# Performance work log

Hardware: AMD Instinct MI355X
Metric: run time of the kernel (lower is better)

## Reference

```python
import jax, jax.numpy as jnp
import numpy as np

TOTAL_NODES = 262144
NUM_GRAPHS = 1024
MAX_NODES = 512
D = 256


def setup_inputs() -> dict:
    key = jax.random.key(0)
    k1, k2 = jax.random.split(key)
    node_emb = jax.random.normal(k1, (TOTAL_NODES, D), dtype=jnp.float32)
    batch_idx = jnp.sort(jax.random.randint(k2, (TOTAL_NODES,), 0, NUM_GRAPHS, dtype=jnp.int64))
    return {"node_emb": node_emb, "batch_idx": batch_idx,
            "num_graphs": NUM_GRAPHS, "max_nodes": MAX_NODES}


def reference(node_emb, batch_idx, num_graphs, max_nodes):
    # counts[g] = number of nodes in graph g  (torch.bincount)
    n = node_emb.shape[0]
    counts = jax.ops.segment_sum(jnp.ones((n,), dtype=jnp.int32), batch_idx,
                                 num_segments=num_graphs)
    # exclusive prefix sum -> start offset of each graph's node block
    starts = jnp.cumsum(counts) - counts
    # position of each node within its graph (batch_idx is sorted)
    pos = jnp.arange(n, dtype=jnp.int32) - starts[batch_idx]
    # single fused scatter replacing the per-graph python loop
    enc_states = jnp.zeros((num_graphs, max_nodes, node_emb.shape[-1]),
                           dtype=node_emb.dtype)
    enc_states = enc_states.at[batch_idx, pos].set(node_emb)
    # mask: first counts[g] slots of each row are 1
    enc_mask = (jnp.arange(max_nodes, dtype=jnp.int32)[None, :]
                < counts[:, None]).astype(jnp.int32)
    return enc_states, enc_mask
```

## Files before the change

### kernel.cpp

```cpp
#include <hip/hip_runtime.h>

#define NUM_GRAPHS 1024
#define MAX_NODES  512
#define DIM        256
#define D4         (DIM / 4)

__global__ void compute_offsets_kernel(const int* __restrict__ bidx32, int n,
                                       int* __restrict__ starts,
                                       int* __restrict__ counts) {
    int g = blockIdx.x * blockDim.x + threadIdx.x;
    if (g >= NUM_GRAPHS) return;
    const bool is64 = (bidx32[n - 1] == 0);

    int lo = 0, hi = n;
    while (lo < hi) {
        int mid = (lo + hi) >> 1;
        int v = is64 ? bidx32[2 * mid] : bidx32[mid];
        if (v < g) lo = mid + 1; else hi = mid;
    }
    int s = lo;

    int g1 = g + 1;
    lo = 0; hi = n;
    while (lo < hi) {
        int mid = (lo + hi) >> 1;
        int v = is64 ? bidx32[2 * mid] : bidx32[mid];
        if (v < g1) lo = mid + 1; else hi = mid;
    }

    starts[g] = s;
    counts[g] = lo - s;
}

__global__ void scatter_states_kernel(const float4* __restrict__ emb,
                                      const int* __restrict__ starts,
                                      const int* __restrict__ counts,
                                      float4* __restrict__ out) {
    const int total = NUM_GRAPHS * MAX_NODES * D4;
    const int stride = gridDim.x * blockDim.x;
    for (int v = blockIdx.x * blockDim.x + threadIdx.x; v < total; v += stride) {
        int row  = v >> 6;
        int lane = v & (D4 - 1);
        int g    = row >> 9;
        int slot = row & (MAX_NODES - 1);
        float4 val = make_float4(0.f, 0.f, 0.f, 0.f);
        if (slot < counts[g]) {
            val = emb[(size_t)(starts[g] + slot) * D4 + lane];
        }
        out[v] = val;
    }
}

__global__ void mask_kernel(const int* __restrict__ counts,
                            float* __restrict__ mask) {
    int idx = blockIdx.x * blockDim.x + threadIdx.x;
    if (idx >= NUM_GRAPHS * MAX_NODES) return;
    int g    = idx >> 9;
    int slot = idx & (MAX_NODES - 1);
    mask[idx] = (slot < counts[g]) ? 1.0f : 0.0f;
}

extern "C" void kernel_launch(void* const* d_in, const int* in_sizes, int n_in,
                              void* d_out, int out_size, void* d_ws, size_t ws_size,
                              hipStream_t stream) {
    const float* node_emb = (const float*)d_in[0];
    const int*   bidx32   = (const int*)d_in[1];
    const int    n        = in_sizes[1];

    int* starts = (int*)d_ws;
    int* counts = starts + NUM_GRAPHS;

    compute_offsets_kernel<<<(NUM_GRAPHS + 255) / 256, 256, 0, stream>>>(
        bidx32, n, starts, counts);

    scatter_states_kernel<<<2048, 256, 0, stream>>>(
        (const float4*)node_emb, starts, counts, (float4*)d_out);

    float* mask = (float*)d_out + (size_t)NUM_GRAPHS * MAX_NODES * DIM;
    mask_kernel<<<(NUM_GRAPHS * MAX_NODES) / 256, 256, 0, stream>>>(counts, mask);
}
```

Before: 206.1 us.

## Fuse mask into scatter, replace binary search with boundary scan, use nontemporal IO

Replaces the per-graph binary-search offset kernel with a per-node boundary-detection kernel that writes start offsets (counts derived as differences). Folds the mask kernel into the scatter kernel, cutting one launch, and fixes the scatter loop to 64 unrolled iterations with constant stride. Uses nontemporal loads/stores for streaming embedding data to reduce cache pollution. The scan launches far more threads, and empty trailing graphs are filled serially by one thread.

After: 188.3 us. -8.6%, faster.

```diff
diff --git a/kernel.cpp b/kernel.cpp
--- a/kernel.cpp
+++ b/kernel.cpp
@@ -4,60 +4,51 @@
 #define MAX_NODES  512
 #define DIM        256
 #define D4         (DIM / 4)
+#define TOTAL_V4   (NUM_GRAPHS * MAX_NODES * D4)
+#define NTHREADS   (2048 * 256)
 
-__global__ void compute_offsets_kernel(const int* __restrict__ bidx32, int n,
-                                       int* __restrict__ starts,
-                                       int* __restrict__ counts) {
-    int g = blockIdx.x * blockDim.x + threadIdx.x;
-    if (g >= NUM_GRAPHS) return;
+typedef float f4 __attribute__((ext_vector_type(4)));
+
+__global__ void scan_offsets_kernel(const int* __restrict__ bidx32, int n,
+                                    int* __restrict__ starts) {
+    int i = blockIdx.x * blockDim.x + threadIdx.x;
+    if (i >= n) return;
     const bool is64 = (bidx32[n - 1] == 0);
-
-    int lo = 0, hi = n;
-    while (lo < hi) {
-        int mid = (lo + hi) >> 1;
-        int v = is64 ? bidx32[2 * mid] : bidx32[mid];
-        if (v < g) lo = mid + 1; else hi = mid;
-    }
-    int s = lo;
-
-    int g1 = g + 1;
-    lo = 0; hi = n;
-    while (lo < hi) {
-        int mid = (lo + hi) >> 1;
-        int v = is64 ? bidx32[2 * mid] : bidx32[mid];
-        if (v < g1) lo = mid + 1; else hi = mid;
-    }
-
-    starts[g] = s;
-    counts[g] = lo - s;
-}
-
-__global__ void scatter_states_kernel(const float4* __restrict__ emb,
-                                      const int* __restrict__ starts,
-                                      const int* __restrict__ counts,
-                                      float4* __restrict__ out) {
-    const int total = NUM_GRAPHS * MAX_NODES * D4;
-    const int stride = gridDim.x * blockDim.x;
-    for (int v = blockIdx.x * blockDim.x + threadIdx.x; v < total; v += stride) {
-        int row  = v >> 6;
-        int lane = v & (D4 - 1);
-        int g    = row >> 9;
-        int slot = row & (MAX_NODES - 1);
-        float4 val = make_float4(0.f, 0.f, 0.f, 0.f);
-        if (slot < counts[g]) {
-            val = emb[(size_t)(starts[g] + slot) * D4 + lane];
-        }
-        out[v] = val;
+    const int cur  = is64 ? bidx32[2 * i] : bidx32[i];
+    const int prev = (i == 0) ? -1 : (is64 ? bidx32[2 * (i - 1)] : bidx32[i - 1]);
+    for (int g = prev + 1; g <= cur; ++g) starts[g] = i;
+    if (i == n - 1) {
+        for (int g = cur + 1; g <= NUM_GRAPHS; ++g) starts[g] = n;
     }
 }
 
-__global__ void mask_kernel(const int* __restrict__ counts,
-                            float* __restrict__ mask) {
-    int idx = blockIdx.x * blockDim.x + threadIdx.x;
-    if (idx >= NUM_GRAPHS * MAX_NODES) return;
-    int g    = idx >> 9;
-    int slot = idx & (MAX_NODES - 1);
-    mask[idx] = (slot < counts[g]) ? 1.0f : 0.0f;
+__global__ void __launch_bounds__(256)
+scatter_states_kernel(const f4* __restrict__ emb,
+                      const int* __restrict__ starts,
+                      f4* __restrict__ out,
+                      float* __restrict__ mask) {
+    const int tid  = blockIdx.x * blockDim.x + threadIdx.x;
+    const int lane = tid & (D4 - 1);
+    const int row0 = tid >> 6;
+    const int slot = row0 & (MAX_NODES - 1);
+    const int g0   = row0 >> 9;
+
+#pragma unroll 8
+    for (int it = 0; it < 64; ++it) {
+        const int g = g0 + it * 16;
+        const int s = starts[g];
+        const int c = starts[g + 1] - s;
+        f4 val = (f4)(0.f);
+        if (slot < c) {
+            val = __builtin_nontemporal_load(&emb[(size_t)(s + slot) * D4 + lane]);
+        }
+        __builtin_nontemporal_store(val, &out[tid + (size_t)it * NTHREADS]);
+    }
+
+    const int mg = tid >> 9;
+    const int ms = tid & (MAX_NODES - 1);
+    const int mc = starts[mg + 1] - starts[mg];
+    __builtin_nontemporal_store((ms < mc) ? 1.0f : 0.0f, &mask[tid]);
 }
 
 extern "C" void kernel_launch(void* const* d_in, const int* in_sizes, int n_in,
@@ -68,14 +59,10 @@
     const int    n        = in_sizes[1];
 
     int* starts = (int*)d_ws;
-    int* counts = starts + NUM_GRAPHS;
 
-    compute_offsets_kernel<<<(NUM_GRAPHS + 255) / 256, 256, 0, stream>>>(
-        bidx32, n, starts, counts);
-
-    scatter_states_kernel<<<2048, 256, 0, stream>>>(
-        (const float4*)node_emb, starts, counts, (float4*)d_out);
+    scan_offsets_kernel<<<(n + 255) / 256, 256, 0, stream>>>(bidx32, n, starts);
 
     float* mask = (float*)d_out + (size_t)NUM_GRAPHS * MAX_NODES * DIM;
-    mask_kernel<<<(NUM_GRAPHS * MAX_NODES) / 256, 256, 0, stream>>>(counts, mask);
+    scatter_states_kernel<<<NTHREADS / 256, 256, 0, stream>>>(
+        (const f4*)node_emb, starts, (f4*)d_out, mask);
 }
```
